# Performance work log

Hardware: AMD Instinct MI355X
Metric: run time of the kernel (lower is better)

Reference implementation:

```python
import jax, jax.numpy as jnp
import numpy as np

BN_EPS = 1e-5


def setup_inputs() -> dict:
    key = jax.random.key(0)
    k1, k2, k3, k4 = jax.random.split(key, 4)
    N, E, D_IN, D_OUT = 100000, 1600000, 128, 128
    x = jax.random.normal(k1, (N, D_IN), dtype=jnp.float32)
    edge_index = jax.random.randint(k2, (2, E), 0, N, dtype=jnp.int64)
    # GCNConv linear (glorot) + bias (zeros init in PyG)
    W = jax.random.normal(k3, (D_OUT, D_IN), dtype=jnp.float32) * (1.0 / np.sqrt(D_IN))
    b = jnp.zeros((D_OUT,), dtype=jnp.float32)
    # BatchNorm affine params
    gamma = jnp.ones((D_OUT,), dtype=jnp.float32)
    beta = jnp.zeros((D_OUT,), dtype=jnp.float32)
    return {"x": x, "edge_index": edge_index, "W": W, "b": b,
            "gamma": gamma, "beta": beta}


def reference(x, edge_index, W, b, gamma, beta):
    N = x.shape[0]
    # --- GCNConv: add self-loops, symmetric normalization ---
    loop = jnp.arange(N, dtype=edge_index.dtype)
    src = jnp.concatenate([edge_index[0], loop])  # [E+N]
    dst = jnp.concatenate([edge_index[1], loop])  # [E+N]
    deg = jax.ops.segment_sum(jnp.ones_like(dst, dtype=x.dtype), dst,
                              num_segments=N)  # in-degree incl. self-loop
    dinv = jnp.where(deg > 0, jax.lax.rsqrt(deg), 0.0)
    norm = dinv[src] * dinv[dst]  # [E+N]
    # linear transform before propagation (PyG GCNConv)
    h = x @ W.T  # [N, D_OUT]
    agg = jax.ops.segment_sum(h[src] * norm[:, None], dst, num_segments=N)
    out = agg + b
    # --- BatchNorm1d (training mode: batch statistics over nodes) ---
    mean = jnp.mean(out, axis=0)
    var = jnp.var(out, axis=0)
    out = (out - mean) * jax.lax.rsqrt(var + BN_EPS) * gamma + beta
    # --- ReLU, residual, dropout(p=0 -> identity) ---
    out = jax.nn.relu(out)
    out = out + x  # residual (in_dim == out_dim)
    return out
```

## Files before the change

### kernel.cpp

```cpp
#include <hip/hip_runtime.h>
#include <hip/hip_fp16.h>

#define BN_EPS 1e-5f

typedef unsigned int uint32;
typedef __attribute__((ext_vector_type(8))) _Float16 f16x8;
typedef __attribute__((ext_vector_type(4))) float f32x4;

union H2U { __half2 h; uint32 u; };

__device__ __forceinline__ __half2 u2h(uint32 u) { H2U c; c.u = u; return c.h; }
__device__ __forceinline__ uint32 h2u(__half2 h) { H2U c; c.h = h; return c.u; }
__device__ __forceinline__ uint32 pack2h(float a, float b) {
    return h2u(__halves2half2(__float2half_rn(a), __float2half_rn(b)));
}
__device__ __forceinline__ float h2lo(uint32 u) {
    return __half2float(__ushort_as_half((unsigned short)(u & 0xffffu)));
}
__device__ __forceinline__ float h2hi(uint32 u) {
    return __half2float(__ushort_as_half((unsigned short)(u >> 16)));
}


__global__ void __launch_bounds__(256) k_prep(const float4* __restrict__ x4, int nx4,
                                              const float4* __restrict__ w4, int nw4,
                                              uint2* __restrict__ xh4, uint2* __restrict__ wh4) {
    int idx = blockIdx.x * 256 + threadIdx.x;
    int stride = gridDim.x * 256;
    for (int i = idx; i < nx4; i += stride) {
        float4 v = x4[i];
        xh4[i] = make_uint2(pack2h(v.x, v.y), pack2h(v.z, v.w));
    }
    for (int i = idx; i < nw4; i += stride) {
        float4 v = w4[i];
        wh4[i] = make_uint2(pack2h(v.x, v.y), pack2h(v.z, v.w));
    }
}


__global__ void __launch_bounds__(256) k_bscatter(const int* __restrict__ ei, int E, int NB,
                                                  int CAP, int* __restrict__ bfill,
                                                  uint32* __restrict__ bpack) {
    __shared__ int h[4][1024];
    int t = threadIdx.x;
    int wave = t >> 6;
    int c0 = (int)((long long)blockIdx.x * E / gridDim.x);
    int c1 = (int)((long long)(blockIdx.x + 1) * E / gridDim.x);
    for (int i = t; i < 4 * 1024; i += 256) h[i >> 10][i & 1023] = 0;
    __syncthreads();
    for (int e = c0 + t; e < c1; e += 256)
        atomicAdd(&h[wave][ei[E + e] >> 8], 1);
    __syncthreads();
    for (int i = t; i < NB; i += 256) {
        int n0 = h[0][i], n1 = h[1][i], n2 = h[2][i], n3 = h[3][i];
        int tot = n0 + n1 + n2 + n3;
        if (tot > 0) {
            int base = i * CAP + atomicAdd(&bfill[i], tot);
            h[0][i] = base;
            h[1][i] = base + n0;
            h[2][i] = base + n0 + n1;
            h[3][i] = base + n0 + n1 + n2;
        }
    }
    __syncthreads();
    for (int e = c0 + t; e < c1; e += 256) {
        int s = ei[e];
        int d = ei[E + e];
        int b = d >> 8;
        int pos = atomicAdd(&h[wave][b], 1);
        bpack[pos] = ((uint32)(d & 255) << 24) | (uint32)s;
    }
}


__global__ void __launch_bounds__(256) k_csr(const uint32* __restrict__ bpack,
                                             const int* __restrict__ bfill, int CAP,
                                             int N,
                                             int* __restrict__ rowptr,
                                             int* __restrict__ rowcnt,
                                             uint32* __restrict__ dpk,
                                             int* __restrict__ col) {
    __shared__ int h[4][256], s[256], cur[4][256];
    int b = blockIdx.x;
    int t = threadIdx.x;
    int wave = t >> 6;
    int e0 = b * CAP, e1 = e0 + bfill[b];
    h[0][t] = 0; h[1][t] = 0; h[2][t] = 0; h[3][t] = 0;
    __syncthreads();
    for (int e = e0 + t; e < e1; e += 256)
        atomicAdd(&h[wave][bpack[e] >> 24], 1);
    __syncthreads();
    int n0 = h[0][t], n1 = h[1][t], n2 = h[2][t], n3 = h[3][t];
    int cnt = n0 + n1 + n2 + n3;
    s[t] = cnt;
    __syncthreads();
    for (int off = 1; off < 256; off <<= 1) {
        int add = (t >= off) ? s[t - off] : 0;
        __syncthreads();
        s[t] += add;
        __syncthreads();
    }
    int excl = s[t] - cnt;
    int node = (b << 8) + t;
    if (node < N) {
        rowptr[node] = e0 + excl;
        rowcnt[node] = cnt;
        float dv = rsqrtf((float)(cnt + 1));
        dpk[node] = pack2h(dv, dv);
    }
    cur[0][t] = e0 + excl;
    cur[1][t] = e0 + excl + n0;
    cur[2][t] = e0 + excl + n0 + n1;
    cur[3][t] = e0 + excl + n0 + n1 + n2;
    __syncthreads();
    for (int e = e0 + t; e < e1; e += 256) {
        uint32 p = bpack[e];
        int pos = atomicAdd(&cur[wave][p >> 24], 1);
        col[pos] = (int)(p & 0xffffffu);
    }
}


#define EDGE_FMA(vv, ww)                                   \
    acc0 = __hfma2(u2h((vv).x), u2h(ww), acc0);            \
    acc1 = __hfma2(u2h((vv).y), u2h(ww), acc1);            \
    acc2 = __hfma2(u2h((vv).z), u2h(ww), acc2);            \
    acc3 = __hfma2(u2h((vv).w), u2h(ww), acc3);

__global__ void __launch_bounds__(256) k_agg(const uint32* __restrict__ xh,
                                             const int* __restrict__ rowptr,
                                             const int* __restrict__ rowcnt,
                                             const int* __restrict__ col,
                                             const uint32* __restrict__ dpk,
                                             uint32* __restrict__ aggh, int N) {
    int wid = blockIdx.x * 4 + (threadIdx.x >> 6);
    if (wid >= N) return;
    int lane = threadIdx.x & 63;
    int g = lane >> 4, c = lane & 15;

    __half2 z = __float2half2_rn(0.f);
    __half2 acc0 = z, acc1 = z, acc2 = z, acc3 = z;

    int e0 = rowptr[wid];
    int e1 = e0 + rowcnt[wid];
    int e = e0;
    for (; e + 16 <= e1; e += 16) {
        int i0 = e + g, i1 = e + 4 + g, i2 = e + 8 + g, i3 = e + 12 + g;
        int s0 = col[i0], s1 = col[i1], s2 = col[i2], s3 = col[i3];
        uint32 w0 = dpk[s0], w1 = dpk[s1], w2 = dpk[s2], w3 = dpk[s3];
        uint4 v0 = *(const uint4*)&xh[(size_t)s0 * 64 + c * 4];
        uint4 v1 = *(const uint4*)&xh[(size_t)s1 * 64 + c * 4];
        uint4 v2 = *(const uint4*)&xh[(size_t)s2 * 64 + c * 4];
        uint4 v3 = *(const uint4*)&xh[(size_t)s3 * 64 + c * 4];
        EDGE_FMA(v0, w0); EDGE_FMA(v1, w1); EDGE_FMA(v2, w2); EDGE_FMA(v3, w3);
    }
    if (e < e1) {
        int i0 = e + g, i1 = e + 4 + g, i2 = e + 8 + g, i3 = e + 12 + g;
        int s0 = 0, s1 = 0, s2 = 0, s3 = 0;
        uint32 w0 = 0, w1 = 0, w2 = 0, w3 = 0;
        if (i0 < e1) { s0 = col[i0]; w0 = dpk[s0]; }
        if (i1 < e1) { s1 = col[i1]; w1 = dpk[s1]; }
        if (i2 < e1) { s2 = col[i2]; w2 = dpk[s2]; }
        if (i3 < e1) { s3 = col[i3]; w3 = dpk[s3]; }
        uint4 v0 = *(const uint4*)&xh[(size_t)s0 * 64 + c * 4];
        uint4 v1 = *(const uint4*)&xh[(size_t)s1 * 64 + c * 4];
        uint4 v2 = *(const uint4*)&xh[(size_t)s2 * 64 + c * 4];
        uint4 v3 = *(const uint4*)&xh[(size_t)s3 * 64 + c * 4];
        EDGE_FMA(v0, w0); EDGE_FMA(v1, w1); EDGE_FMA(v2, w2); EDGE_FMA(v3, w3);
    }
    uint32 u;
    u = __shfl_xor(h2u(acc0), 16); acc0 = __hadd2(acc0, u2h(u));
    u = __shfl_xor(h2u(acc0), 32); acc0 = __hadd2(acc0, u2h(u));
    u = __shfl_xor(h2u(acc1), 16); acc1 = __hadd2(acc1, u2h(u));
    u = __shfl_xor(h2u(acc1), 32); acc1 = __hadd2(acc1, u2h(u));
    u = __shfl_xor(h2u(acc2), 16); acc2 = __hadd2(acc2, u2h(u));
    u = __shfl_xor(h2u(acc2), 32); acc2 = __hadd2(acc2, u2h(u));
    u = __shfl_xor(h2u(acc3), 16); acc3 = __hadd2(acc3, u2h(u));
    u = __shfl_xor(h2u(acc3), 32); acc3 = __hadd2(acc3, u2h(u));

    if (g == 0) {
        float di = h2lo(dpk[wid]);
        uint4 sv = *(const uint4*)&xh[(size_t)wid * 64 + c * 4];
        uint4 o;
        o.x = pack2h(di * (di * h2lo(sv.x) + __low2float(acc0)),
                     di * (di * h2hi(sv.x) + __high2float(acc0)));
        o.y = pack2h(di * (di * h2lo(sv.y) + __low2float(acc1)),
                     di * (di * h2hi(sv.y) + __high2float(acc1)));
        o.z = pack2h(di * (di * h2lo(sv.z) + __low2float(acc2)),
                     di * (di * h2hi(sv.z) + __high2float(acc2)));
        o.w = pack2h(di * (di * h2lo(sv.w) + __low2float(acc3)),
                     di * (di * h2hi(sv.w) + __high2float(acc3)));
        *(uint4*)&aggh[(size_t)wid * 64 + c * 4] = o;
    }
}


#define STAGE_W()                                                            \
    for (int m = threadIdx.x; m < 2048; m += 256) {                          \
        int row = m >> 4, cc = m & 15;                                       \
        uint4 v = *(const uint4*)&Wh[row * 128 + cc * 8];                    \
        *(uint4*)((char*)wlds + row * 256 + ((cc * 16) ^ ((row & 7) << 4))) = v; \
    }

#define MFMA_TILE(acc, tile)                                                 \
    {                                                                        \
        int arow = (tile) * 64 + wave * 16 + lrow;                           \
        bool avalid = arow < N;                                              \
        _Pragma("unroll")                                                    \
        for (int kc = 0; kc < 4; ++kc) {                                     \
            f16x8 a;                                                         \
            if (avalid) a = *(const f16x8*)&Ah[(size_t)arow * 128 + kc * 32 + g * 8]; \
            else        a = (f16x8){0, 0, 0, 0, 0, 0, 0, 0};                 \
            _Pragma("unroll")                                                \
            for (int ct = 0; ct < 8; ++ct) {                                 \
                int row = ct * 16 + lrow;                                    \
                const f16x8 bfr = *(const f16x8*)((const char*)wlds + row * 256 \
                                   + ((kc * 64 + g * 16) ^ ((row & 7) << 4))); \
                acc[ct] = __builtin_amdgcn_mfma_f32_16x16x32_f16(a, bfr, acc[ct], 0, 0, 0); \
            }                                                                \
        }                                                                    \
    }

__global__ void __launch_bounds__(256) k_gemm_stats(const _Float16* __restrict__ Ah,
                                                    const _Float16* __restrict__ Wh,
                                                    const float* __restrict__ bias,
                                                    int N, int ntiles,
                                                    float* __restrict__ partials) {
    __shared__ uint32 wlds[8192];
    __shared__ float red[1024];
    STAGE_W();
    __syncthreads();

    int t = threadIdx.x;
    int wave = t >> 6, lane = t & 63;
    int lrow = lane & 15, g = lane >> 4;

    float bv[8];
    #pragma unroll
    for (int ct = 0; ct < 8; ++ct) bv[ct] = bias[ct * 16 + lrow];

    float s[8], sq[8];
    #pragma unroll
    for (int ct = 0; ct < 8; ++ct) { s[ct] = 0.f; sq[ct] = 0.f; }

    for (int tile = blockIdx.x; tile < ntiles; tile += gridDim.x) {
        f32x4 acc[8];
        #pragma unroll
        for (int ct = 0; ct < 8; ++ct) acc[ct] = (f32x4){0.f, 0.f, 0.f, 0.f};
        MFMA_TILE(acc, tile);
        int orow0 = tile * 64 + wave * 16 + g * 4;
        #pragma unroll
        for (int ct = 0; ct < 8; ++ct) {
            #pragma unroll
            for (int rr = 0; rr < 4; ++rr) {
                if (orow0 + rr < N) {
                    float o = acc[ct][rr] + bv[ct];
                    s[ct] += o; sq[ct] += o * o;
                }
            }
        }
    }
    #pragma unroll
    for (int ct = 0; ct < 8; ++ct) {
        s[ct] += __shfl_xor(s[ct], 16); sq[ct] += __shfl_xor(sq[ct], 16);
        s[ct] += __shfl_xor(s[ct], 32); sq[ct] += __shfl_xor(sq[ct], 32);
    }
    if (lane < 16) {
        #pragma unroll
        for (int ct = 0; ct < 8; ++ct) {
            int colI = ct * 16 + lrow;
            red[wave * 256 + colI] = s[ct];
            red[wave * 256 + 128 + colI] = sq[ct];
        }
    }
    __syncthreads();
    if (t < 256)
        partials[blockIdx.x * 256 + t] = red[t] + red[256 + t] + red[512 + t] + red[768 + t];
}


__global__ void __launch_bounds__(1024) k_bnparams(const float* __restrict__ partials, int nblk,
                                                   const float* __restrict__ gamma,
                                                   const float* __restrict__ beta,
                                                   float invN, float* __restrict__ ss) {
    __shared__ float red[1024];
    int tid = threadIdx.x;
    int colI = tid & 255, q = tid >> 8;
    int bq = nblk >> 2;
    float v0 = 0.f, v1 = 0.f, v2 = 0.f, v3 = 0.f;
    int b0 = q * bq;
    for (int b = b0; b < b0 + bq; b += 4) {
        v0 += partials[(b + 0) * 256 + colI];
        v1 += partials[(b + 1) * 256 + colI];
        v2 += partials[(b + 2) * 256 + colI];
        v3 += partials[(b + 3) * 256 + colI];
    }
    red[q * 256 + colI] = (v0 + v1) + (v2 + v3);
    __syncthreads();
    if (tid < 256) {
        float tot = red[tid] + red[256 + tid] + red[512 + tid] + red[768 + tid];
        red[tid] = tot;
    }
    __syncthreads();
    if (tid < 128) {
        float mean = red[tid] * invN;
        float var = red[128 + tid] * invN - mean * mean;
        float sc = gamma[tid] * rsqrtf(var + BN_EPS);
        ss[tid] = sc;
        ss[128 + tid] = beta[tid] - mean * sc;
    }
}

__global__ void __launch_bounds__(256) k_gemm_apply(const _Float16* __restrict__ Ah,
                                                    const _Float16* __restrict__ Wh,
                                                    const float* __restrict__ bias,
                                                    const float* __restrict__ ss,
                                                    const uint32* __restrict__ xh,
                                                    int N, int ntiles,
                                                    float* __restrict__ out) {
    __shared__ uint32 wlds[8192];
    STAGE_W();
    __syncthreads();

    int t = threadIdx.x;
    int wave = t >> 6, lane = t & 63;
    int lrow = lane & 15, g = lane >> 4;

    float bv[8], scv[8], shv[8];
    #pragma unroll
    for (int ct = 0; ct < 8; ++ct) {
        int colI = ct * 16 + lrow;
        bv[ct] = bias[colI]; scv[ct] = ss[colI]; shv[ct] = ss[128 + colI];
    }

    for (int tile = blockIdx.x; tile < ntiles; tile += gridDim.x) {
        f32x4 acc[8];
        #pragma unroll
        for (int ct = 0; ct < 8; ++ct) acc[ct] = (f32x4){0.f, 0.f, 0.f, 0.f};
        MFMA_TILE(acc, tile);
        int orow0 = tile * 64 + wave * 16 + g * 4;
        #pragma unroll
        for (int ct = 0; ct < 8; ++ct) {
            int ocol = ct * 16 + lrow;
            #pragma unroll
            for (int rr = 0; rr < 4; ++rr) {
                int r = orow0 + rr;
                if (r < N) {
                    float pre = acc[ct][rr] + bv[ct];
                    float o = fmaxf(pre * scv[ct] + shv[ct], 0.f);
                    uint32 xv = xh[(size_t)r * 64 + (ocol >> 1)];
                    float xr = (ocol & 1) ? h2hi(xv) : h2lo(xv);
                    out[(size_t)r * 128 + ocol] = o + xr;
                }
            }
        }
    }
}


extern "C" void kernel_launch(void* const* d_in, const int* in_sizes, int n_in,
                              void* d_out, int out_size, void* d_ws, size_t ws_size,
                              hipStream_t stream) {
    const float* x     = (const float*)d_in[0];
    const int*   ei    = (const int*)d_in[1];
    const float* W     = (const float*)d_in[2];
    const float* bias  = (const float*)d_in[3];
    const float* gamma = (const float*)d_in[4];
    const float* beta  = (const float*)d_in[5];
    float* out = (float*)d_out;

    const int D = 128;
    int N = in_sizes[0] / D;
    int E = in_sizes[1] / 2;
    int NB = (N + 255) >> 8;
    int CAP = ((E + NB - 1) / NB + 1024 + 63) & ~63;

    const int GSTATS = 256;
    const int GAPPLY = 512;

    char* ws = (char*)d_ws;
    size_t off = 0;
    auto alloc = [&](size_t bytes) -> void* {
        void* p = ws + off;
        off += (bytes + 255) & ~(size_t)255;
        return p;
    };
    uint32* xh   = (uint32*)alloc((size_t)N * 64 * sizeof(uint32));
    uint32* aggh = (uint32*)alloc((size_t)N * 64 * sizeof(uint32));
    uint32* bpack= (uint32*)alloc((size_t)NB * CAP * sizeof(uint32));
    int* col     = (int*)alloc((size_t)NB * CAP * sizeof(int));
    _Float16* Wh = (_Float16*)alloc((size_t)D * D * sizeof(_Float16));
    int* rowptr  = (int*)alloc((size_t)N * sizeof(int));
    int* rowcnt  = (int*)alloc((size_t)N * sizeof(int));
    uint32* dpk  = (uint32*)alloc((size_t)N * sizeof(uint32));
    float* ss    = (float*)alloc(256 * sizeof(float));
    float* partials = (float*)alloc((size_t)GSTATS * 256 * sizeof(float));
    int* bfill   = (int*)alloc(1024 * sizeof(int));

    hipMemsetAsync(bfill, 0, 1024 * sizeof(int), stream);

    k_prep<<<2048, 256, 0, stream>>>((const float4*)x, N * 32, (const float4*)W, D * D / 4,
                                     (uint2*)xh, (uint2*)Wh);
    k_bscatter<<<256, 256, 0, stream>>>(ei, E, NB, CAP, bfill, bpack);
    k_csr<<<NB, 256, 0, stream>>>(bpack, bfill, CAP, N, rowptr, rowcnt, dpk, col);
    k_agg<<<(N + 3) / 4, 256, 0, stream>>>(xh, rowptr, rowcnt, col, dpk, aggh, N);

    int ntiles = (N + 63) / 64;
    k_gemm_stats<<<GSTATS, 256, 0, stream>>>((const _Float16*)aggh, Wh, bias, N, ntiles, partials);
    k_bnparams<<<1, 1024, 0, stream>>>(partials, GSTATS, gamma, beta, 1.0f / (float)N, ss);
    k_gemm_apply<<<GAPPLY, 256, 0, stream>>>((const _Float16*)aggh, Wh, bias, ss, xh, N, ntiles, out);
}
```

Measured before the change: 181.1 us.

## Fuse aggregation with stats GEMM and merge prep with edge bucketing

Aggregation is folded into the BN-statistics GEMM kernel. Each block gathers a 64-node tile into LDS, writes it to aggh, and runs the MFMA stats pass on the LDS copy, so the stats kernel no longer re-reads aggh from global memory. The fp16 conversion of x and W is merged with the edge bucket scatter into one launch, with separate block ranges for each job. In exchange, the fused kernel processes 16 nodes per wave in sequence with far fewer blocks than the old one-wave-per-node launch. That cuts memory-level parallelism in the latency-bound gather, and the per-block LDS footprint also rises.

```diff
diff --git a/kernel.cpp b/kernel.cpp
--- a/kernel.cpp
+++ b/kernel.cpp
@@ -22,53 +22,54 @@
 }
 
 
-__global__ void __launch_bounds__(256) k_prep(const float4* __restrict__ x4, int nx4,
-                                              const float4* __restrict__ w4, int nw4,
-                                              uint2* __restrict__ xh4, uint2* __restrict__ wh4) {
-    int idx = blockIdx.x * 256 + threadIdx.x;
-    int stride = gridDim.x * 256;
-    for (int i = idx; i < nx4; i += stride) {
-        float4 v = x4[i];
-        xh4[i] = make_uint2(pack2h(v.x, v.y), pack2h(v.z, v.w));
-    }
-    for (int i = idx; i < nw4; i += stride) {
-        float4 v = w4[i];
-        wh4[i] = make_uint2(pack2h(v.x, v.y), pack2h(v.z, v.w));
-    }
-}
-
-
-__global__ void __launch_bounds__(256) k_bscatter(const int* __restrict__ ei, int E, int NB,
-                                                  int CAP, int* __restrict__ bfill,
-                                                  uint32* __restrict__ bpack) {
-    __shared__ int h[4][1024];
+__global__ void __launch_bounds__(256) k_prep_scatter(const float4* __restrict__ x4, int nx4,
+                                                      const float4* __restrict__ w4, int nw4,
+                                                      uint2* __restrict__ xh4, uint2* __restrict__ wh4,
+                                                      const int* __restrict__ ei, int E, int NB,
+                                                      int CAP, int* __restrict__ bfill,
+                                                      uint32* __restrict__ bpack) {
     int t = threadIdx.x;
-    int wave = t >> 6;
-    int c0 = (int)((long long)blockIdx.x * E / gridDim.x);
-    int c1 = (int)((long long)(blockIdx.x + 1) * E / gridDim.x);
-    for (int i = t; i < 4 * 1024; i += 256) h[i >> 10][i & 1023] = 0;
-    __syncthreads();
-    for (int e = c0 + t; e < c1; e += 256)
-        atomicAdd(&h[wave][ei[E + e] >> 8], 1);
-    __syncthreads();
-    for (int i = t; i < NB; i += 256) {
-        int n0 = h[0][i], n1 = h[1][i], n2 = h[2][i], n3 = h[3][i];
-        int tot = n0 + n1 + n2 + n3;
-        if (tot > 0) {
-            int base = i * CAP + atomicAdd(&bfill[i], tot);
-            h[0][i] = base;
-            h[1][i] = base + n0;
-            h[2][i] = base + n0 + n1;
-            h[3][i] = base + n0 + n1 + n2;
-        }
-    }
-    __syncthreads();
-    for (int e = c0 + t; e < c1; e += 256) {
-        int s = ei[e];
-        int d = ei[E + e];
-        int b = d >> 8;
-        int pos = atomicAdd(&h[wave][b], 1);
-        bpack[pos] = ((uint32)(d & 255) << 24) | (uint32)s;
+    if (blockIdx.x < 256) {
+        __shared__ int h[4][1024];
+        int wave = t >> 6;
+        int c0 = (int)((long long)blockIdx.x * E / 256);
+        int c1 = (int)((long long)(blockIdx.x + 1) * E / 256);
+        for (int i = t; i < 4 * 1024; i += 256) h[i >> 10][i & 1023] = 0;
+        __syncthreads();
+        for (int e = c0 + t; e < c1; e += 256)
+            atomicAdd(&h[wave][ei[E + e] >> 8], 1);
+        __syncthreads();
+        for (int i = t; i < NB; i += 256) {
+            int n0 = h[0][i], n1 = h[1][i], n2 = h[2][i], n3 = h[3][i];
+            int tot = n0 + n1 + n2 + n3;
+            if (tot > 0) {
+                int base = i * CAP + atomicAdd(&bfill[i], tot);
+                h[0][i] = base;
+                h[1][i] = base + n0;
+                h[2][i] = base + n0 + n1;
+                h[3][i] = base + n0 + n1 + n2;
+            }
+        }
+        __syncthreads();
+        for (int e = c0 + t; e < c1; e += 256) {
+            int s = ei[e];
+            int d = ei[E + e];
+            int b = d >> 8;
+            int pos = atomicAdd(&h[wave][b], 1);
+            bpack[pos] = ((uint32)(d & 255) << 24) | (uint32)s;
+        }
+    } else {
+        int nb = gridDim.x - 256;
+        int idx = (blockIdx.x - 256) * 256 + t;
+        int stride = nb * 256;
+        for (int i = idx; i < nx4; i += stride) {
+            float4 v = x4[i];
+            xh4[i] = make_uint2(pack2h(v.x, v.y), pack2h(v.z, v.w));
+        }
+        for (int i = idx; i < nw4; i += stride) {
+            float4 v = w4[i];
+            wh4[i] = make_uint2(pack2h(v.x, v.y), pack2h(v.z, v.w));
+        }
     }
 }
 
@@ -127,80 +128,189 @@
     acc2 = __hfma2(u2h((vv).z), u2h(ww), acc2);            \
     acc3 = __hfma2(u2h((vv).w), u2h(ww), acc3);
 
-__global__ void __launch_bounds__(256) k_agg(const uint32* __restrict__ xh,
-                                             const int* __restrict__ rowptr,
-                                             const int* __restrict__ rowcnt,
-                                             const int* __restrict__ col,
-                                             const uint32* __restrict__ dpk,
-                                             uint32* __restrict__ aggh, int N) {
-    int wid = blockIdx.x * 4 + (threadIdx.x >> 6);
-    if (wid >= N) return;
-    int lane = threadIdx.x & 63;
-    int g = lane >> 4, c = lane & 15;
-
-    __half2 z = __float2half2_rn(0.f);
-    __half2 acc0 = z, acc1 = z, acc2 = z, acc3 = z;
-
-    int e0 = rowptr[wid];
-    int e1 = e0 + rowcnt[wid];
-    int e = e0;
-    for (; e + 16 <= e1; e += 16) {
-        int i0 = e + g, i1 = e + 4 + g, i2 = e + 8 + g, i3 = e + 12 + g;
-        int s0 = col[i0], s1 = col[i1], s2 = col[i2], s3 = col[i3];
-        uint32 w0 = dpk[s0], w1 = dpk[s1], w2 = dpk[s2], w3 = dpk[s3];
-        uint4 v0 = *(const uint4*)&xh[(size_t)s0 * 64 + c * 4];
-        uint4 v1 = *(const uint4*)&xh[(size_t)s1 * 64 + c * 4];
-        uint4 v2 = *(const uint4*)&xh[(size_t)s2 * 64 + c * 4];
-        uint4 v3 = *(const uint4*)&xh[(size_t)s3 * 64 + c * 4];
-        EDGE_FMA(v0, w0); EDGE_FMA(v1, w1); EDGE_FMA(v2, w2); EDGE_FMA(v3, w3);
-    }
-    if (e < e1) {
-        int i0 = e + g, i1 = e + 4 + g, i2 = e + 8 + g, i3 = e + 12 + g;
-        int s0 = 0, s1 = 0, s2 = 0, s3 = 0;
-        uint32 w0 = 0, w1 = 0, w2 = 0, w3 = 0;
-        if (i0 < e1) { s0 = col[i0]; w0 = dpk[s0]; }
-        if (i1 < e1) { s1 = col[i1]; w1 = dpk[s1]; }
-        if (i2 < e1) { s2 = col[i2]; w2 = dpk[s2]; }
-        if (i3 < e1) { s3 = col[i3]; w3 = dpk[s3]; }
-        uint4 v0 = *(const uint4*)&xh[(size_t)s0 * 64 + c * 4];
-        uint4 v1 = *(const uint4*)&xh[(size_t)s1 * 64 + c * 4];
-        uint4 v2 = *(const uint4*)&xh[(size_t)s2 * 64 + c * 4];
-        uint4 v3 = *(const uint4*)&xh[(size_t)s3 * 64 + c * 4];
-        EDGE_FMA(v0, w0); EDGE_FMA(v1, w1); EDGE_FMA(v2, w2); EDGE_FMA(v3, w3);
-    }
-    uint32 u;
-    u = __shfl_xor(h2u(acc0), 16); acc0 = __hadd2(acc0, u2h(u));
-    u = __shfl_xor(h2u(acc0), 32); acc0 = __hadd2(acc0, u2h(u));
-    u = __shfl_xor(h2u(acc1), 16); acc1 = __hadd2(acc1, u2h(u));
-    u = __shfl_xor(h2u(acc1), 32); acc1 = __hadd2(acc1, u2h(u));
-    u = __shfl_xor(h2u(acc2), 16); acc2 = __hadd2(acc2, u2h(u));
-    u = __shfl_xor(h2u(acc2), 32); acc2 = __hadd2(acc2, u2h(u));
-    u = __shfl_xor(h2u(acc3), 16); acc3 = __hadd2(acc3, u2h(u));
-    u = __shfl_xor(h2u(acc3), 32); acc3 = __hadd2(acc3, u2h(u));
-
-    if (g == 0) {
-        float di = h2lo(dpk[wid]);
-        uint4 sv = *(const uint4*)&xh[(size_t)wid * 64 + c * 4];
-        uint4 o;
-        o.x = pack2h(di * (di * h2lo(sv.x) + __low2float(acc0)),
-                     di * (di * h2hi(sv.x) + __high2float(acc0)));
-        o.y = pack2h(di * (di * h2lo(sv.y) + __low2float(acc1)),
-                     di * (di * h2hi(sv.y) + __high2float(acc1)));
-        o.z = pack2h(di * (di * h2lo(sv.z) + __low2float(acc2)),
-                     di * (di * h2hi(sv.z) + __high2float(acc2)));
-        o.w = pack2h(di * (di * h2lo(sv.w) + __low2float(acc3)),
-                     di * (di * h2hi(sv.w) + __high2float(acc3)));
-        *(uint4*)&aggh[(size_t)wid * 64 + c * 4] = o;
-    }
-}
-
-
 #define STAGE_W()                                                            \
     for (int m = threadIdx.x; m < 2048; m += 256) {                          \
         int row = m >> 4, cc = m & 15;                                       \
         uint4 v = *(const uint4*)&Wh[row * 128 + cc * 8];                    \
         *(uint4*)((char*)wlds + row * 256 + ((cc * 16) ^ ((row & 7) << 4))) = v; \
     }
+
+__global__ void __launch_bounds__(256) k_agg_stats(const uint32* __restrict__ xh,
+                                                   const int* __restrict__ rowptr,
+                                                   const int* __restrict__ rowcnt,
+                                                   const int* __restrict__ col,
+                                                   const uint32* __restrict__ dpk,
+                                                   const _Float16* __restrict__ Wh,
+                                                   const float* __restrict__ bias,
+                                                   uint32* __restrict__ aggh,
+                                                   int N, int ntiles,
+                                                   float* __restrict__ partials) {
+    __shared__ uint32 wlds[8192];
+    __shared__ uint32 atile[4096];
+    __shared__ float red[1024];
+
+    STAGE_W();
+
+    int t = threadIdx.x;
+    int wave = t >> 6, lane = t & 63;
+    int g = lane >> 4, c = lane & 15;
+    int lrow = lane & 15;
+
+    float bv[8];
+    #pragma unroll
+    for (int ct = 0; ct < 8; ++ct) bv[ct] = bias[ct * 16 + lrow];
+
+    float s[8], sq[8];
+    #pragma unroll
+    for (int ct = 0; ct < 8; ++ct) { s[ct] = 0.f; sq[ct] = 0.f; }
+
+    __syncthreads();
+
+    for (int tile = blockIdx.x; tile < ntiles; tile += gridDim.x) {
+        for (int i = 0; i < 16; ++i) {
+            int node = tile * 64 + wave * 16 + i;
+            int arow = wave * 16 + i;
+            if (node < N) {
+                __half2 z = __float2half2_rn(0.f);
+                __half2 acc0 = z, acc1 = z, acc2 = z, acc3 = z;
+                int e0 = rowptr[node];
+                int e1 = e0 + rowcnt[node];
+                int e = e0;
+                for (; e + 16 <= e1; e += 16) {
+                    int i0 = e + g, i1 = e + 4 + g, i2 = e + 8 + g, i3 = e + 12 + g;
+                    int s0 = col[i0], s1 = col[i1], s2 = col[i2], s3 = col[i3];
+                    uint32 w0 = dpk[s0], w1 = dpk[s1], w2 = dpk[s2], w3 = dpk[s3];
+                    uint4 v0 = *(const uint4*)&xh[(size_t)s0 * 64 + c * 4];
+                    uint4 v1 = *(const uint4*)&xh[(size_t)s1 * 64 + c * 4];
+                    uint4 v2 = *(const uint4*)&xh[(size_t)s2 * 64 + c * 4];
+                    uint4 v3 = *(const uint4*)&xh[(size_t)s3 * 64 + c * 4];
+                    EDGE_FMA(v0, w0); EDGE_FMA(v1, w1); EDGE_FMA(v2, w2); EDGE_FMA(v3, w3);
+                }
+                if (e < e1) {
+                    int i0 = e + g, i1 = e + 4 + g, i2 = e + 8 + g, i3 = e + 12 + g;
+                    int s0 = 0, s1 = 0, s2 = 0, s3 = 0;
+                    uint32 w0 = 0, w1 = 0, w2 = 0, w3 = 0;
+                    if (i0 < e1) { s0 = col[i0]; w0 = dpk[s0]; }
+                    if (i1 < e1) { s1 = col[i1]; w1 = dpk[s1]; }
+                    if (i2 < e1) { s2 = col[i2]; w2 = dpk[s2]; }
+                    if (i3 < e1) { s3 = col[i3]; w3 = dpk[s3]; }
+                    uint4 v0 = *(const uint4*)&xh[(size_t)s0 * 64 + c * 4];
+                    uint4 v1 = *(const uint4*)&xh[(size_t)s1 * 64 + c * 4];
+                    uint4 v2 = *(const uint4*)&xh[(size_t)s2 * 64 + c * 4];
+                    uint4 v3 = *(const uint4*)&xh[(size_t)s3 * 64 + c * 4];
+                    EDGE_FMA(v0, w0); EDGE_FMA(v1, w1); EDGE_FMA(v2, w2); EDGE_FMA(v3, w3);
+                }
+                uint32 u;
+                u = __shfl_xor(h2u(acc0), 16); acc0 = __hadd2(acc0, u2h(u));
+                u = __shfl_xor(h2u(acc0), 32); acc0 = __hadd2(acc0, u2h(u));
+                u = __shfl_xor(h2u(acc1), 16); acc1 = __hadd2(acc1, u2h(u));
+                u = __shfl_xor(h2u(acc1), 32); acc1 = __hadd2(acc1, u2h(u));
+                u = __shfl_xor(h2u(acc2), 16); acc2 = __hadd2(acc2, u2h(u));
+                u = __shfl_xor(h2u(acc2), 32); acc2 = __hadd2(acc2, u2h(u));
+                u = __shfl_xor(h2u(acc3), 16); acc3 = __hadd2(acc3, u2h(u));
+                u = __shfl_xor(h2u(acc3), 32); acc3 = __hadd2(acc3, u2h(u));
+                if (g == 0) {
+                    float di = h2lo(dpk[node]);
+                    uint4 sv = *(const uint4*)&xh[(size_t)node * 64 + c * 4];
+                    uint4 o;
+                    o.x = pack2h(di * (di * h2lo(sv.x) + __low2float(acc0)),
+                                 di * (di * h2hi(sv.x) + __high2float(acc0)));
+                    o.y = pack2h(di * (di * h2lo(sv.y) + __low2float(acc1)),
+                                 di * (di * h2hi(sv.y) + __high2float(acc1)));
+                    o.z = pack2h(di * (di * h2lo(sv.z) + __low2float(acc2)),
+                                 di * (di * h2hi(sv.z) + __high2float(acc2)));
+                    o.w = pack2h(di * (di * h2lo(sv.w) + __low2float(acc3)),
+                                 di * (di * h2hi(sv.w) + __high2float(acc3)));
+                    *(uint4*)&aggh[(size_t)node * 64 + c * 4] = o;
+                    *(uint4*)((char*)atile + arow * 256 + ((c * 16) ^ ((arow & 7) << 4))) = o;
+                }
+            } else if (g == 0) {
+                *(uint4*)((char*)atile + arow * 256 + ((c * 16) ^ ((arow & 7) << 4))) =
+                    make_uint4(0, 0, 0, 0);
+            }
+        }
+        __syncthreads();
+        f32x4 acc[8];
+        #pragma unroll
+        for (int ct = 0; ct < 8; ++ct) acc[ct] = (f32x4){0.f, 0.f, 0.f, 0.f};
+        #pragma unroll
+        for (int kc = 0; kc < 4; ++kc) {
+            int arow = wave * 16 + lrow;
+            f16x8 a = *(const f16x8*)((const char*)atile + arow * 256
+                        + ((kc * 64 + g * 16) ^ ((arow & 7) << 4)));
+            #pragma unroll
+            for (int ct = 0; ct < 8; ++ct) {
+                int row = ct * 16 + lrow;
+                const f16x8 bfr = *(const f16x8*)((const char*)wlds + row * 256
+                                    + ((kc * 64 + g * 16) ^ ((row & 7) << 4)));
+                acc[ct] = __builtin_amdgcn_mfma_f32_16x16x32_f16(a, bfr, acc[ct], 0, 0, 0);
+            }
+        }
+        int orow0 = tile * 64 + wave * 16 + g * 4;
+        #pragma unroll
+        for (int ct = 0; ct < 8; ++ct) {
+            #pragma unroll
+            for (int rr = 0; rr < 4; ++rr) {
+                if (orow0 + rr < N) {
+                    float o = acc[ct][rr] + bv[ct];
+                    s[ct] += o; sq[ct] += o * o;
+                }
+            }
+        }
+        __syncthreads();
+    }
+
+    #pragma unroll
+    for (int ct = 0; ct < 8; ++ct) {
+        s[ct] += __shfl_xor(s[ct], 16); sq[ct] += __shfl_xor(sq[ct], 16);
+        s[ct] += __shfl_xor(s[ct], 32); sq[ct] += __shfl_xor(sq[ct], 32);
+    }
+    if (lane < 16) {
+        #pragma unroll
+        for (int ct = 0; ct < 8; ++ct) {
+            int colI = ct * 16 + lrow;
+            red[wave * 256 + colI] = s[ct];
+            red[wave * 256 + 128 + colI] = sq[ct];
+        }
+    }
+    __syncthreads();
+    if (t < 256)
+        partials[blockIdx.x * 256 + t] = red[t] + red[256 + t] + red[512 + t] + red[768 + t];
+}
+
+
+__global__ void __launch_bounds__(1024) k_bnparams(const float* __restrict__ partials, int nblk,
+                                                   const float* __restrict__ gamma,
+                                                   const float* __restrict__ beta,
+                                                   float invN, float* __restrict__ ss) {
+    __shared__ float red[1024];
+    int tid = threadIdx.x;
+    int colI = tid & 255, q = tid >> 8;
+    int bq = nblk >> 2;
+    float v0 = 0.f, v1 = 0.f, v2 = 0.f, v3 = 0.f;
+    int b0 = q * bq;
+    for (int b = b0; b < b0 + bq; b += 4) {
+        v0 += partials[(b + 0) * 256 + colI];
+        v1 += partials[(b + 1) * 256 + colI];
+        v2 += partials[(b + 2) * 256 + colI];
+        v3 += partials[(b + 3) * 256 + colI];
+    }
+    red[q * 256 + colI] = (v0 + v1) + (v2 + v3);
+    __syncthreads();
+    if (tid < 256) {
+        float tot = red[tid] + red[256 + tid] + red[512 + tid] + red[768 + tid];
+        red[tid] = tot;
+    }
+    __syncthreads();
+    if (tid < 128) {
+        float mean = red[tid] * invN;
+        float var = red[128 + tid] * invN - mean * mean;
+        float sc = gamma[tid] * rsqrtf(var + BN_EPS);
+        ss[tid] = sc;
+        ss[128 + tid] = beta[tid] - mean * sc;
+    }
+}
+
 
 #define MFMA_TILE(acc, tile)                                                 \
     {                                                                        \
@@ -221,96 +331,6 @@
         }                                                                    \
     }
 
-__global__ void __launch_bounds__(256) k_gemm_stats(const _Float16* __restrict__ Ah,
-                                                    const _Float16* __restrict__ Wh,
-                                                    const float* __restrict__ bias,
-                                                    int N, int ntiles,
-                                                    float* __restrict__ partials) {
-    __shared__ uint32 wlds[8192];
-    __shared__ float red[1024];
-    STAGE_W();
-    __syncthreads();
-
-    int t = threadIdx.x;
-    int wave = t >> 6, lane = t & 63;
-    int lrow = lane & 15, g = lane >> 4;
-
-    float bv[8];
-    #pragma unroll
-    for (int ct = 0; ct < 8; ++ct) bv[ct] = bias[ct * 16 + lrow];
-
-    float s[8], sq[8];
-    #pragma unroll
-    for (int ct = 0; ct < 8; ++ct) { s[ct] = 0.f; sq[ct] = 0.f; }
-
-    for (int tile = blockIdx.x; tile < ntiles; tile += gridDim.x) {
-        f32x4 acc[8];
-        #pragma unroll
-        for (int ct = 0; ct < 8; ++ct) acc[ct] = (f32x4){0.f, 0.f, 0.f, 0.f};
-        MFMA_TILE(acc, tile);
-        int orow0 = tile * 64 + wave * 16 + g * 4;
-        #pragma unroll
-        for (int ct = 0; ct < 8; ++ct) {
-            #pragma unroll
-            for (int rr = 0; rr < 4; ++rr) {
-                if (orow0 + rr < N) {
-                    float o = acc[ct][rr] + bv[ct];
-                    s[ct] += o; sq[ct] += o * o;
-                }
-            }
-        }
-    }
-    #pragma unroll
-    for (int ct = 0; ct < 8; ++ct) {
-        s[ct] += __shfl_xor(s[ct], 16); sq[ct] += __shfl_xor(sq[ct], 16);
-        s[ct] += __shfl_xor(s[ct], 32); sq[ct] += __shfl_xor(sq[ct], 32);
-    }
-    if (lane < 16) {
-        #pragma unroll
-        for (int ct = 0; ct < 8; ++ct) {
-            int colI = ct * 16 + lrow;
-            red[wave * 256 + colI] = s[ct];
-            red[wave * 256 + 128 + colI] = sq[ct];
-        }
-    }
-    __syncthreads();
-    if (t < 256)
-        partials[blockIdx.x * 256 + t] = red[t] + red[256 + t] + red[512 + t] + red[768 + t];
-}
-
-
-__global__ void __launch_bounds__(1024) k_bnparams(const float* __restrict__ partials, int nblk,
-                                                   const float* __restrict__ gamma,
-                                                   const float* __restrict__ beta,
-                                                   float invN, float* __restrict__ ss) {
-    __shared__ float red[1024];
-    int tid = threadIdx.x;
-    int colI = tid & 255, q = tid >> 8;
-    int bq = nblk >> 2;
-    float v0 = 0.f, v1 = 0.f, v2 = 0.f, v3 = 0.f;
-    int b0 = q * bq;
-    for (int b = b0; b < b0 + bq; b += 4) {
-        v0 += partials[(b + 0) * 256 + colI];
-        v1 += partials[(b + 1) * 256 + colI];
-        v2 += partials[(b + 2) * 256 + colI];
-        v3 += partials[(b + 3) * 256 + colI];
-    }
-    red[q * 256 + colI] = (v0 + v1) + (v2 + v3);
-    __syncthreads();
-    if (tid < 256) {
-        float tot = red[tid] + red[256 + tid] + red[512 + tid] + red[768 + tid];
-        red[tid] = tot;
-    }
-    __syncthreads();
-    if (tid < 128) {
-        float mean = red[tid] * invN;
-        float var = red[128 + tid] * invN - mean * mean;
-        float sc = gamma[tid] * rsqrtf(var + BN_EPS);
-        ss[tid] = sc;
-        ss[128 + tid] = beta[tid] - mean * sc;
-    }
-}
-
 __global__ void __launch_bounds__(256) k_gemm_apply(const _Float16* __restrict__ Ah,
                                                     const _Float16* __restrict__ Wh,
                                                     const float* __restrict__ bias,
@@ -375,7 +395,7 @@
     int NB = (N + 255) >> 8;
     int CAP = ((E + NB - 1) / NB + 1024 + 63) & ~63;
 
-    const int GSTATS = 256;
+    const int GAGG = 1024;
     const int GAPPLY = 512;
 
     char* ws = (char*)d_ws;
@@ -394,19 +414,22 @@
     int* rowcnt  = (int*)alloc((size_t)N * sizeof(int));
     uint32* dpk  = (uint32*)alloc((size_t)N * sizeof(uint32));
     float* ss    = (float*)alloc(256 * sizeof(float));
-    float* partials = (float*)alloc((size_t)GSTATS * 256 * sizeof(float));
+    float* partials = (float*)alloc((size_t)GAGG * 256 * sizeof(float));
     int* bfill   = (int*)alloc(1024 * sizeof(int));
 
     hipMemsetAsync(bfill, 0, 1024 * sizeof(int), stream);
 
-    k_prep<<<2048, 256, 0, stream>>>((const float4*)x, N * 32, (const float4*)W, D * D / 4,
-                                     (uint2*)xh, (uint2*)Wh);
-    k_bscatter<<<256, 256, 0, stream>>>(ei, E, NB, CAP, bfill, bpack);
+    k_prep_scatter<<<2048, 256, 0, stream>>>((const float4*)x, N * 32,
+                                             (const float4*)W, D * D / 4,
+                                             (uint2*)xh, (uint2*)Wh,
+                                             ei, E, NB, CAP, bfill, bpack);
     k_csr<<<NB, 256, 0, stream>>>(bpack, bfill, CAP, N, rowptr, rowcnt, dpk, col);
-    k_agg<<<(N + 3) / 4, 256, 0, stream>>>(xh, rowptr, rowcnt, col, dpk, aggh, N);
 
     int ntiles = (N + 63) / 64;
-    k_gemm_stats<<<GSTATS, 256, 0, stream>>>((const _Float16*)aggh, Wh, bias, N, ntiles, partials);
-    k_bnparams<<<1, 1024, 0, stream>>>(partials, GSTATS, gamma, beta, 1.0f / (float)N, ss);
-    k_gemm_apply<<<GAPPLY, 256, 0, stream>>>((const _Float16*)aggh, Wh, bias, ss, xh, N, ntiles, out);
-}
+    k_agg_stats<<<GAGG, 256, 0, stream>>>(xh, rowptr, rowcnt, col, dpk,
+                                          (const _Float16*)Wh, bias, aggh,
+                                          N, ntiles, partials);
+    k_bnparams<<<1, 1024, 0, stream>>>(partials, GAGG, gamma, beta, 1.0f / (float)N, ss);
+    k_gemm_apply<<<GAPPLY, 256, 0, stream>>>((const _Float16*)aggh, (const _Float16*)Wh,
+                                             bias, ss, xh, N, ntiles, out);
+}
```

Measured after the change: 237.6 us. 31.2% more time.
